# Kernel optimization log

Measured on AMD Instinct MI355X. Metric: run time of the kernel, lower is better.

Reference implementation:

```python
import jax, jax.numpy as jnp
import numpy as np

N, F_IN, HID, E, G = 100000, 256, 256, 800000, 256


def setup_inputs() -> dict:
    key = jax.random.key(0)
    ks = jax.random.split(key, 10)
    x = jax.random.normal(ks[0], (N, F_IN), dtype=jnp.float32)
    edge_index = jax.random.randint(ks[1], (2, E), 0, N, dtype=jnp.int64)
    batch = jnp.sort(jax.random.randint(ks[2], (N,), 0, G, dtype=jnp.int64))
    s = 1.0 / np.sqrt(HID)
    W1 = jax.random.normal(ks[3], (F_IN, HID), dtype=jnp.float32) * s
    b1 = jnp.zeros((HID,), dtype=jnp.float32)
    W2 = jax.random.normal(ks[4], (HID, HID), dtype=jnp.float32) * s
    b2 = jnp.zeros((HID,), dtype=jnp.float32)
    Wc1 = jax.random.normal(ks[5], (HID, HID // 2), dtype=jnp.float32) * s
    bc1 = jnp.zeros((HID // 2,), dtype=jnp.float32)
    Wc2 = jax.random.normal(ks[6], (HID // 2, 2), dtype=jnp.float32) * s
    bc2 = jnp.zeros((2,), dtype=jnp.float32)
    return dict(x=x, edge_index=edge_index, batch=batch, num_graphs=G,
                W1=W1, b1=b1, W2=W2, b2=b2, Wc1=Wc1, bc1=bc1, Wc2=Wc2, bc2=bc2)


def _gcn_layer(h, src, dst, inv_sqrt_deg, W, b):
    # GCNConv: D^-1/2 (A + I) D^-1/2 (h W) + b
    hw = h @ W                                            # (N, H)
    coef = inv_sqrt_deg[src] * inv_sqrt_deg[dst]          # (E,)
    msgs = hw[src] * coef[:, None]                        # (E, H)
    agg = jax.ops.segment_sum(msgs, dst, num_segments=h.shape[0])
    self_loop = hw * (inv_sqrt_deg * inv_sqrt_deg)[:, None]
    return agg + self_loop + b


def reference(x, edge_index, batch, num_graphs, W1, b1, W2, b2, Wc1, bc1, Wc2, bc2):
    n = x.shape[0]
    src, dst = edge_index[0], edge_index[1]
    # degree with self-loops (symmetric normalization)
    deg = jax.ops.segment_sum(jnp.ones((src.shape[0],), jnp.float32), dst,
                              num_segments=n) + 1.0
    inv_sqrt_deg = jax.lax.rsqrt(deg)

    h = jax.nn.relu(_gcn_layer(x, src, dst, inv_sqrt_deg, W1, b1))
    node_emb = jax.nn.relu(_gcn_layer(h, src, dst, inv_sqrt_deg, W2, b2))

    # per-graph mean pooling (segment mean replacing the Python loop)
    sums = jax.ops.segment_sum(node_emb, batch, num_segments=num_graphs)
    counts = jax.ops.segment_sum(jnp.ones((n,), jnp.float32), batch,
                                 num_segments=num_graphs)
    graph_emb = sums / jnp.maximum(counts, 1.0)[:, None]

    # classifier MLP (dropout is identity in eval mode)
    hcls = jax.nn.relu(graph_emb @ Wc1 + bc1)
    logits = hcls @ Wc2 + bc2                             # (G, 2)
    return logits, node_emb
```

## Files before the change

kernel.cpp:

```cpp
#include <hip/hip_runtime.h>
#include <hip/hip_bf16.h>

#define HID 256
#define NGRAPH 256

typedef __bf16 bf16_t;
typedef __attribute__((ext_vector_type(8))) __bf16 bf16x8;
typedef __attribute__((ext_vector_type(4))) __bf16 bf16x4;
typedef __attribute__((ext_vector_type(4))) float f32x4;

__global__ void zero_int_kernel(int* __restrict__ p, int n) {
    int i = blockIdx.x * blockDim.x + threadIdx.x;
    if (i < n) p[i] = 0;
}

__global__ void count_deg_kernel(const int* __restrict__ ei, int E, int* __restrict__ deg) {
    int e = blockIdx.x * blockDim.x + threadIdx.x;
    if (e >= E) return;
    int dst = ei[E + e];
    atomicAdd(&deg[dst], 1);
}

#define SCHUNK 512

__global__ __launch_bounds__(256) void scan_pass1_kernel(
    const int* __restrict__ deg, int N, int* __restrict__ bsum) {
    __shared__ int red[256];
    int b = blockIdx.x, t = threadIdx.x;
    int i0 = b * SCHUNK + 2 * t;
    int v = 0;
    if (i0 < N) v += deg[i0];
    if (i0 + 1 < N) v += deg[i0 + 1];
    red[t] = v;
    __syncthreads();
    for (int s = 128; s > 0; s >>= 1) {
        if (t < s) red[t] += red[t + s];
        __syncthreads();
    }
    if (t == 0) bsum[b] = red[0];
}

__global__ __launch_bounds__(256) void scan_pass2_kernel(
    const int* __restrict__ bsum, int NB, int* __restrict__ boff) {
    __shared__ int s[256];
    int t = threadIdx.x;
    int v = (t < NB) ? bsum[t] : 0;
    s[t] = v;
    __syncthreads();
    for (int off = 1; off < 256; off <<= 1) {
        int x = s[t];
        if (t >= off) x += s[t - off];
        __syncthreads();
        s[t] = x;
        __syncthreads();
    }
    if (t < NB) boff[t] = s[t] - v;
}

__global__ __launch_bounds__(256) void scan_pass3_kernel(
    const int* __restrict__ deg, int N, const int* __restrict__ boff,
    int* __restrict__ rowptr, int* __restrict__ cursor, float* __restrict__ invd) {
    __shared__ int s[256];
    int b = blockIdx.x, t = threadIdx.x;
    int i0 = b * SCHUNK + 2 * t;
    int d0 = (i0 < N) ? deg[i0] : 0;
    int d1 = (i0 + 1 < N) ? deg[i0 + 1] : 0;
    int pair = d0 + d1;
    s[t] = pair;
    __syncthreads();
    for (int off = 1; off < 256; off <<= 1) {
        int x = s[t];
        if (t >= off) x += s[t - off];
        __syncthreads();
        s[t] = x;
        __syncthreads();
    }
    int excl = s[t] - pair + boff[b];
    if (i0 < N) {
        rowptr[i0] = excl;
        cursor[i0] = excl;
        invd[i0] = rsqrtf((float)d0 + 1.0f);
    }
    if (i0 + 1 < N) {
        int e1 = excl + d0;
        rowptr[i0 + 1] = e1;
        cursor[i0 + 1] = e1;
        invd[i0 + 1] = rsqrtf((float)d1 + 1.0f);
    }
}

__global__ void fill_csr_kernel(const int* __restrict__ ei, int E,
                                int* __restrict__ cursor, int* __restrict__ csr_src) {
    int e = blockIdx.x * blockDim.x + threadIdx.x;
    if (e >= E) return;
    int src = ei[e];
    int dst = ei[E + e];
    int pos = atomicAdd(&cursor[dst], 1);
    csr_src[pos] = src;
}

__global__ __launch_bounds__(256) void wsplit_kernel(
    const float* __restrict__ W, bf16_t* __restrict__ Wf) {
    int idx = blockIdx.x * 256 + threadIdx.x;
    float w = W[idx];
    int k = idx >> 8, n = idx & 255;
    int k0 = k >> 5, kg = (k >> 3) & 3, j = k & 7;
    int nt = n >> 4, m = n & 15;
    Wf[(size_t)(((k0 * 16 + nt) * 64) + kg * 16 + m) * 8 + j] = (bf16_t)w;
}

#define GBM 64

template <int SPLIT>
__global__ __launch_bounds__(256, 2) void gemm_mfma_kernel(
    const void* __restrict__ Xv, const bf16_t* __restrict__ Wf,
    const float* __restrict__ rowscale, bf16_t* __restrict__ out, int Nrows) {
    __shared__ bf16_t Blds[32768];

    const int tid = threadIdx.x;
    const int wave = tid >> 6;
    const int lane = tid & 63;
    const int row0 = blockIdx.x * GBM;
    const int m = lane & 15;
    const int kg = lane >> 4;

    const int arow_raw = row0 + wave * 16 + m;
    const int arow = (arow_raw < Nrows) ? arow_raw : 0;

    f32x4 acc[16];
#pragma unroll
    for (int i = 0; i < 16; ++i) acc[i] = (f32x4){0.f, 0.f, 0.f, 0.f};

#pragma unroll
    for (int c = 0; c < 2; ++c) {
        float4 xa0, xb0, xa1, xb1, xa2, xb2, xa3, xb3;
        bf16x8 ah0, ah1, ah2, ah3;
        if (SPLIT) {
            const float* xr = (const float*)Xv + (size_t)arow * 256 + c * 128 + kg * 8;
            xa0 = *(const float4*)&xr[0];   xb0 = *(const float4*)&xr[4];
            xa1 = *(const float4*)&xr[32];  xb1 = *(const float4*)&xr[36];
            xa2 = *(const float4*)&xr[64];  xb2 = *(const float4*)&xr[68];
            xa3 = *(const float4*)&xr[96];  xb3 = *(const float4*)&xr[100];
        } else {
            const bf16_t* xr = (const bf16_t*)Xv + (size_t)arow * 256 + c * 128 + kg * 8;
            ah0 = *(const bf16x8*)&xr[0];
            ah1 = *(const bf16x8*)&xr[32];
            ah2 = *(const bf16x8*)&xr[64];
            ah3 = *(const bf16x8*)&xr[96];
        }

        if (c) __syncthreads();
#pragma unroll
        for (int it = 0; it < 16; ++it)
            *(bf16x8*)&Blds[it * 2048 + tid * 8] =
                *(const bf16x8*)&Wf[c * 32768 + it * 2048 + tid * 8];
        __syncthreads();

#pragma unroll
        for (int k0c = 0; k0c < 4; ++k0c) {
            bf16x8 ah, al;
            if (SPLIT) {
                float4 xa = (k0c == 0) ? xa0 : (k0c == 1) ? xa1 : (k0c == 2) ? xa2 : xa3;
                float4 xb = (k0c == 0) ? xb0 : (k0c == 1) ? xb1 : (k0c == 2) ? xb2 : xb3;
                float xf[8] = {xa.x, xa.y, xa.z, xa.w, xb.x, xb.y, xb.z, xb.w};
#pragma unroll
                for (int q = 0; q < 8; ++q) {
                    bf16_t hi = (bf16_t)xf[q];
                    ah[q] = hi;
                    al[q] = (bf16_t)(xf[q] - (float)hi);
                }
            } else {
                ah = (k0c == 0) ? ah0 : (k0c == 1) ? ah1 : (k0c == 2) ? ah2 : ah3;
            }
            bf16x8 bh[16];
#pragma unroll
            for (int nt = 0; nt < 16; ++nt)
                bh[nt] = *(const bf16x8*)&Blds[(k0c * 16 + nt) * 512 + lane * 8];
#pragma unroll
            for (int nt = 0; nt < 16; ++nt) {
                acc[nt] = __builtin_amdgcn_mfma_f32_16x16x32_bf16(ah, bh[nt], acc[nt], 0, 0, 0);
                if (SPLIT)
                    acc[nt] = __builtin_amdgcn_mfma_f32_16x16x32_bf16(al, bh[nt], acc[nt], 0, 0, 0);
            }
        }
    }

    const int rbase = row0 + wave * 16 + kg * 4;
#pragma unroll
    for (int j = 0; j < 4; ++j) {
        int r = rbase + j;
        if (r < Nrows) {
            float sc = rowscale[r];
#pragma unroll
            for (int nt = 0; nt < 16; ++nt)
                out[(size_t)r * 256 + nt * 16 + m] = (bf16_t)(acc[nt][j] * sc);
        }
    }
}

template <typename OutT>
__global__ __launch_bounds__(256) void gcn_aggregate_kernel(
    const bf16_t* __restrict__ hs, const int* __restrict__ rowptr,
    const int* __restrict__ deg, const int* __restrict__ csr_src,
    const float* __restrict__ inv_d, const float* __restrict__ bias,
    OutT* __restrict__ out, int N) {
    int gwid = (blockIdx.x * blockDim.x + threadIdx.x) >> 6;
    int lane = threadIdx.x & 63;
    if (gwid >= N) return;
    int base = rowptr[gwid];
    int len = deg[gwid];
    int c = lane * 4;

    bf16x4 sv = *(const bf16x4*)&hs[(size_t)gwid * 256 + c];
    float ax0 = (float)sv[0], ay0 = (float)sv[1], az0 = (float)sv[2], aw0 = (float)sv[3];
    float ax1 = 0.f, ay1 = 0.f, az1 = 0.f, aw1 = 0.f;
    float ax2 = 0.f, ay2 = 0.f, az2 = 0.f, aw2 = 0.f;
    float ax3 = 0.f, ay3 = 0.f, az3 = 0.f, aw3 = 0.f;
    int i = 0;
    for (; i + 4 <= len; i += 4) {
        int s0 = csr_src[base + i];
        int s1 = csr_src[base + i + 1];
        int s2 = csr_src[base + i + 2];
        int s3 = csr_src[base + i + 3];
        bf16x4 v0 = *(const bf16x4*)&hs[(size_t)s0 * 256 + c];
        bf16x4 v1 = *(const bf16x4*)&hs[(size_t)s1 * 256 + c];
        bf16x4 v2 = *(const bf16x4*)&hs[(size_t)s2 * 256 + c];
        bf16x4 v3 = *(const bf16x4*)&hs[(size_t)s3 * 256 + c];
        ax0 += (float)v0[0]; ay0 += (float)v0[1]; az0 += (float)v0[2]; aw0 += (float)v0[3];
        ax1 += (float)v1[0]; ay1 += (float)v1[1]; az1 += (float)v1[2]; aw1 += (float)v1[3];
        ax2 += (float)v2[0]; ay2 += (float)v2[1]; az2 += (float)v2[2]; aw2 += (float)v2[3];
        ax3 += (float)v3[0]; ay3 += (float)v3[1]; az3 += (float)v3[2]; aw3 += (float)v3[3];
    }
    for (; i < len; ++i) {
        int s = csr_src[base + i];
        bf16x4 v = *(const bf16x4*)&hs[(size_t)s * 256 + c];
        ax0 += (float)v[0]; ay0 += (float)v[1]; az0 += (float)v[2]; aw0 += (float)v[3];
    }
    float ax = (ax0 + ax1) + (ax2 + ax3);
    float ay = (ay0 + ay1) + (ay2 + ay3);
    float az = (az0 + az1) + (az2 + az3);
    float aw = (aw0 + aw1) + (aw2 + aw3);

    float sc = inv_d[gwid];
    float4 bb = *(const float4*)&bias[c];
    float ox = fmaxf(fmaf(ax, sc, bb.x), 0.f);
    float oy = fmaxf(fmaf(ay, sc, bb.y), 0.f);
    float oz = fmaxf(fmaf(az, sc, bb.z), 0.f);
    float ow = fmaxf(fmaf(aw, sc, bb.w), 0.f);
    if constexpr (sizeof(OutT) == 2) {
        bf16x4 o;
        o[0] = (bf16_t)ox; o[1] = (bf16_t)oy; o[2] = (bf16_t)oz; o[3] = (bf16_t)ow;
        *(bf16x4*)&out[(size_t)gwid * 256 + c] = o;
    } else {
        float4 o = {ox, oy, oz, ow};
        *(float4*)&out[(size_t)gwid * 256 + c] = o;
    }
}

__global__ void graph_bounds_kernel(const int* __restrict__ batch, int N, int G,
                                    int* __restrict__ gstart) {
    int i = blockIdx.x * blockDim.x + threadIdx.x;
    if (i > N) return;
    int cur = (i < N) ? batch[i] : G;
    int prev = (i == 0) ? -1 : batch[i - 1];
    for (int g = prev + 1; g <= cur; ++g) gstart[g] = i;
}

__global__ __launch_bounds__(256) void pool_mean_kernel(
    const float* __restrict__ emb, const int* __restrict__ gstart,
    float* __restrict__ gemb) {
    int g = blockIdx.x;
    int j = threadIdx.x;
    int s = gstart[g], e = gstart[g + 1];
    float s0 = 0.f, s1 = 0.f, s2 = 0.f, s3 = 0.f;
    int n = s;
    for (; n + 4 <= e; n += 4) {
        s0 += emb[(size_t)n * 256 + j];
        s1 += emb[(size_t)(n + 1) * 256 + j];
        s2 += emb[(size_t)(n + 2) * 256 + j];
        s3 += emb[(size_t)(n + 3) * 256 + j];
    }
    for (; n < e; ++n) s0 += emb[(size_t)n * 256 + j];
    float sum = (s0 + s1) + (s2 + s3);
    float cnt = fmaxf((float)(e - s), 1.0f);
    gemb[g * 256 + j] = sum / cnt;
}

__global__ __launch_bounds__(128) void cls1_kernel(
    const float* __restrict__ gemb, const float* __restrict__ Wc1,
    const float* __restrict__ bc1, float* __restrict__ hcls) {
    int g = blockIdx.x;
    int j = threadIdx.x;
    float sum = bc1[j];
    for (int k = 0; k < 256; ++k) sum = fmaf(gemb[g * 256 + k], Wc1[k * 128 + j], sum);
    hcls[g * 128 + j] = fmaxf(sum, 0.f);
}

__global__ void cls2_kernel(const float* __restrict__ hcls, const float* __restrict__ Wc2,
                            const float* __restrict__ bc2, float* __restrict__ logits, int G) {
    int idx = blockIdx.x * blockDim.x + threadIdx.x;
    if (idx >= G * 2) return;
    int g = idx >> 1, c = idx & 1;
    float sum = bc2[c];
    for (int k = 0; k < 128; ++k) sum = fmaf(hcls[g * 128 + k], Wc2[k * 2 + c], sum);
    logits[idx] = sum;
}

extern "C" void kernel_launch(void* const* d_in, const int* in_sizes, int n_in,
                              void* d_out, int out_size, void* d_ws, size_t ws_size,
                              hipStream_t stream) {
    const float* x   = (const float*)d_in[0];
    const int*   ei  = (const int*)d_in[1];
    const int*   batch = (const int*)d_in[2];
    const float* W1  = (const float*)d_in[4];
    const float* b1  = (const float*)d_in[5];
    const float* W2  = (const float*)d_in[6];
    const float* b2  = (const float*)d_in[7];
    const float* Wc1 = (const float*)d_in[8];
    const float* bc1 = (const float*)d_in[9];
    const float* Wc2 = (const float*)d_in[10];
    const float* bc2 = (const float*)d_in[11];

    const int N = in_sizes[0] / HID;
    const int E = in_sizes[1] / 2;
    const int G = NGRAPH;

    float* logits   = (float*)d_out;
    float* node_out = (float*)d_out + (size_t)G * 2;

    char* wsb = (char*)d_ws;
    size_t off = 0;
    auto alloc = [&](size_t bytes) -> void* {
        void* p = wsb + off;
        off += (bytes + 255) & ~(size_t)255;
        return p;
    };
    bf16_t* hs     = (bf16_t*)alloc((size_t)N * HID * 2);
    bf16_t* hb     = (bf16_t*)alloc((size_t)N * HID * 2);
    int*    rowptr = (int*)alloc((size_t)N * 4);
    int*    cursor = (int*)alloc((size_t)N * 4);
    int*    degi   = (int*)alloc((size_t)N * 4);
    int*    csr    = (int*)alloc((size_t)E * 4);
    float*  invd   = (float*)alloc((size_t)N * 4);
    int*    gstart = (int*)alloc((size_t)(G + 1) * 4);
    float*  gemb   = (float*)alloc((size_t)G * HID * 4);
    float*  hcls   = (float*)alloc((size_t)G * (HID / 2) * 4);
    int*    bsum   = (int*)alloc(256 * 4);
    int*    boff   = (int*)alloc(256 * 4);
    bf16_t* wf     = (bf16_t*)alloc((size_t)HID * HID * 2);
    (void)ws_size; (void)n_in; (void)out_size;

    const int NB = (N + SCHUNK - 1) / SCHUNK;

    zero_int_kernel<<<(N + 255) / 256, 256, 0, stream>>>(degi, N);
    count_deg_kernel<<<(E + 255) / 256, 256, 0, stream>>>(ei, E, degi);
    scan_pass1_kernel<<<NB, 256, 0, stream>>>(degi, N, bsum);
    scan_pass2_kernel<<<1, 256, 0, stream>>>(bsum, NB, boff);
    scan_pass3_kernel<<<NB, 256, 0, stream>>>(degi, N, boff, rowptr, cursor, invd);
    fill_csr_kernel<<<(E + 255) / 256, 256, 0, stream>>>(ei, E, cursor, csr);

    const int GB = (N + GBM - 1) / GBM;

    wsplit_kernel<<<HID * HID / 256, 256, 0, stream>>>(W1, wf);
    gemm_mfma_kernel<1><<<GB, 256, 0, stream>>>(x, wf, invd, hs, N);
    gcn_aggregate_kernel<bf16_t><<<(N * 64 + 255) / 256, 256, 0, stream>>>(
        hs, rowptr, degi, csr, invd, b1, hb, N);

    wsplit_kernel<<<HID * HID / 256, 256, 0, stream>>>(W2, wf);
    gemm_mfma_kernel<0><<<GB, 256, 0, stream>>>(hb, wf, invd, hs, N);
    gcn_aggregate_kernel<float><<<(N * 64 + 255) / 256, 256, 0, stream>>>(
        hs, rowptr, degi, csr, invd, b2, node_out, N);

    graph_bounds_kernel<<<(N + 1 + 255) / 256, 256, 0, stream>>>(batch, N, G, gstart);
    pool_mean_kernel<<<G, 256, 0, stream>>>(node_out, gstart, gemb);
    cls1_kernel<<<G, 128, 0, stream>>>(gemb, Wc1, bc1, hcls);
    cls2_kernel<<<(G * 2 + 255) / 256, 256, 0, stream>>>(hcls, Wc2, bc2, logits, G);
}
```

Measured before the change: 383.0 us.

## Enlarge GEMM tiles, unroll aggregation by eight, split pooling across column blocks

The GEMM moves to 128-row tiles with 512 threads, so each shared-memory load of W serves more rows, and B fragments are now loaded just before each MFMA instead of held in a 16-entry register array, lowering register pressure. The aggregation kernel gains an 8-way unrolled gather loop to keep more independent loads in flight per wave. Pooling now splits each graph over 4 column blocks, with 4 row groups per block combined through shared memory, to raise parallelism from 256 blocks. The larger launch bound and the per-iteration LDS loads could serialise LDS reads with MFMAs, and the 4-per-CU occupancy target may not be reachable.

```diff
diff --git a/kernel.cpp b/kernel.cpp
--- a/kernel.cpp
+++ b/kernel.cpp
@@ -109,10 +109,10 @@
     Wf[(size_t)(((k0 * 16 + nt) * 64) + kg * 16 + m) * 8 + j] = (bf16_t)w;
 }
 
-#define GBM 64
+#define GBM 128
 
 template <int SPLIT>
-__global__ __launch_bounds__(256, 2) void gemm_mfma_kernel(
+__global__ __launch_bounds__(512, 4) void gemm_mfma_kernel(
     const void* __restrict__ Xv, const bf16_t* __restrict__ Wf,
     const float* __restrict__ rowscale, bf16_t* __restrict__ out, int Nrows) {
     __shared__ bf16_t Blds[32768];
@@ -151,9 +151,9 @@
 
         if (c) __syncthreads();
 #pragma unroll
-        for (int it = 0; it < 16; ++it)
-            *(bf16x8*)&Blds[it * 2048 + tid * 8] =
-                *(const bf16x8*)&Wf[c * 32768 + it * 2048 + tid * 8];
+        for (int it = 0; it < 8; ++it)
+            *(bf16x8*)&Blds[it * 4096 + tid * 8] =
+                *(const bf16x8*)&Wf[c * 32768 + it * 4096 + tid * 8];
         __syncthreads();
 
 #pragma unroll
@@ -172,15 +172,12 @@
             } else {
                 ah = (k0c == 0) ? ah0 : (k0c == 1) ? ah1 : (k0c == 2) ? ah2 : ah3;
             }
-            bf16x8 bh[16];
-#pragma unroll
-            for (int nt = 0; nt < 16; ++nt)
-                bh[nt] = *(const bf16x8*)&Blds[(k0c * 16 + nt) * 512 + lane * 8];
 #pragma unroll
             for (int nt = 0; nt < 16; ++nt) {
-                acc[nt] = __builtin_amdgcn_mfma_f32_16x16x32_bf16(ah, bh[nt], acc[nt], 0, 0, 0);
+                bf16x8 bh = *(const bf16x8*)&Blds[(k0c * 16 + nt) * 512 + lane * 8];
+                acc[nt] = __builtin_amdgcn_mfma_f32_16x16x32_bf16(ah, bh, acc[nt], 0, 0, 0);
                 if (SPLIT)
-                    acc[nt] = __builtin_amdgcn_mfma_f32_16x16x32_bf16(al, bh[nt], acc[nt], 0, 0, 0);
+                    acc[nt] = __builtin_amdgcn_mfma_f32_16x16x32_bf16(al, bh, acc[nt], 0, 0, 0);
             }
         }
     }
@@ -217,6 +214,32 @@
     float ax2 = 0.f, ay2 = 0.f, az2 = 0.f, aw2 = 0.f;
     float ax3 = 0.f, ay3 = 0.f, az3 = 0.f, aw3 = 0.f;
     int i = 0;
+    for (; i + 8 <= len; i += 8) {
+        int s0 = csr_src[base + i];
+        int s1 = csr_src[base + i + 1];
+        int s2 = csr_src[base + i + 2];
+        int s3 = csr_src[base + i + 3];
+        int s4 = csr_src[base + i + 4];
+        int s5 = csr_src[base + i + 5];
+        int s6 = csr_src[base + i + 6];
+        int s7 = csr_src[base + i + 7];
+        bf16x4 v0 = *(const bf16x4*)&hs[(size_t)s0 * 256 + c];
+        bf16x4 v1 = *(const bf16x4*)&hs[(size_t)s1 * 256 + c];
+        bf16x4 v2 = *(const bf16x4*)&hs[(size_t)s2 * 256 + c];
+        bf16x4 v3 = *(const bf16x4*)&hs[(size_t)s3 * 256 + c];
+        bf16x4 v4 = *(const bf16x4*)&hs[(size_t)s4 * 256 + c];
+        bf16x4 v5 = *(const bf16x4*)&hs[(size_t)s5 * 256 + c];
+        bf16x4 v6 = *(const bf16x4*)&hs[(size_t)s6 * 256 + c];
+        bf16x4 v7 = *(const bf16x4*)&hs[(size_t)s7 * 256 + c];
+        ax0 += (float)v0[0] + (float)v4[0]; ay0 += (float)v0[1] + (float)v4[1];
+        az0 += (float)v0[2] + (float)v4[2]; aw0 += (float)v0[3] + (float)v4[3];
+        ax1 += (float)v1[0] + (float)v5[0]; ay1 += (float)v1[1] + (float)v5[1];
+        az1 += (float)v1[2] + (float)v5[2]; aw1 += (float)v1[3] + (float)v5[3];
+        ax2 += (float)v2[0] + (float)v6[0]; ay2 += (float)v2[1] + (float)v6[1];
+        az2 += (float)v2[2] + (float)v6[2]; aw2 += (float)v2[3] + (float)v6[3];
+        ax3 += (float)v3[0] + (float)v7[0]; ay3 += (float)v3[1] + (float)v7[1];
+        az3 += (float)v3[2] + (float)v7[2]; aw3 += (float)v3[3] + (float)v7[3];
+    }
     for (; i + 4 <= len; i += 4) {
         int s0 = csr_src[base + i];
         int s1 = csr_src[base + i + 1];
@@ -269,21 +292,21 @@
 __global__ __launch_bounds__(256) void pool_mean_kernel(
     const float* __restrict__ emb, const int* __restrict__ gstart,
     float* __restrict__ gemb) {
+    __shared__ float red[4][64];
     int g = blockIdx.x;
-    int j = threadIdx.x;
+    int col = blockIdx.y * 64 + (threadIdx.x & 63);
+    int rg = threadIdx.x >> 6;
     int s = gstart[g], e = gstart[g + 1];
-    float s0 = 0.f, s1 = 0.f, s2 = 0.f, s3 = 0.f;
-    int n = s;
-    for (; n + 4 <= e; n += 4) {
-        s0 += emb[(size_t)n * 256 + j];
-        s1 += emb[(size_t)(n + 1) * 256 + j];
-        s2 += emb[(size_t)(n + 2) * 256 + j];
-        s3 += emb[(size_t)(n + 3) * 256 + j];
-    }
-    for (; n < e; ++n) s0 += emb[(size_t)n * 256 + j];
-    float sum = (s0 + s1) + (s2 + s3);
-    float cnt = fmaxf((float)(e - s), 1.0f);
-    gemb[g * 256 + j] = sum / cnt;
+    float sum = 0.f;
+    for (int n = s + rg; n < e; n += 4) sum += emb[(size_t)n * 256 + col];
+    red[rg][threadIdx.x & 63] = sum;
+    __syncthreads();
+    if (rg == 0) {
+        int l = threadIdx.x & 63;
+        float t = (red[0][l] + red[1][l]) + (red[2][l] + red[3][l]);
+        float cnt = fmaxf((float)(e - s), 1.0f);
+        gemb[g * 256 + col] = t / cnt;
+    }
 }
 
 __global__ __launch_bounds__(128) void cls1_kernel(
@@ -362,17 +385,17 @@
     const int GB = (N + GBM - 1) / GBM;
 
     wsplit_kernel<<<HID * HID / 256, 256, 0, stream>>>(W1, wf);
-    gemm_mfma_kernel<1><<<GB, 256, 0, stream>>>(x, wf, invd, hs, N);
+    gemm_mfma_kernel<1><<<GB, 512, 0, stream>>>(x, wf, invd, hs, N);
     gcn_aggregate_kernel<bf16_t><<<(N * 64 + 255) / 256, 256, 0, stream>>>(
         hs, rowptr, degi, csr, invd, b1, hb, N);
 
     wsplit_kernel<<<HID * HID / 256, 256, 0, stream>>>(W2, wf);
-    gemm_mfma_kernel<0><<<GB, 256, 0, stream>>>(hb, wf, invd, hs, N);
+    gemm_mfma_kernel<0><<<GB, 512, 0, stream>>>(hb, wf, invd, hs, N);
     gcn_aggregate_kernel<float><<<(N * 64 + 255) / 256, 256, 0, stream>>>(
         hs, rowptr, degi, csr, invd, b2, node_out, N);
 
     graph_bounds_kernel<<<(N + 1 + 255) / 256, 256, 0, stream>>>(batch, N, G, gstart);
-    pool_mean_kernel<<<G, 256, 0, stream>>>(node_out, gstart, gemb);
+    pool_mean_kernel<<<dim3(G, 4), 256, 0, stream>>>(node_out, gstart, gemb);
     cls1_kernel<<<G, 128, 0, stream>>>(gemb, Wc1, bc1, hcls);
     cls2_kernel<<<(G * 2 + 255) / 256, 256, 0, stream>>>(hcls, Wc2, bc2, logits, G);
 }
```

New measurement: 383.5 us. Within noise of the previous version (+0.1%).
